# Kernel optimization log

Hardware: AMD Instinct MI355X
Metric: run time of the kernel (lower is better)

The kernel has to match this reference:

```python
import jax, jax.numpy as jnp
import numpy as np

N_WIN = 8      # windows per side (j = i = n_win)
NUM_HEADS = 8
TOPK = 4


def setup_inputs() -> dict:
    key = jax.random.key(0)
    k1, k2 = jax.random.split(key)
    cv_feature = jax.random.normal(k1, (1, 128, 128, 256), dtype=jnp.float32)
    mv_feature = jax.random.normal(k2, (1, 4, 128, 128, 256), dtype=jnp.float32)
    return {"cv_feature": cv_feature, "mv_feature": mv_feature}


def reference(cv_feature, mv_feature):
    n, H, W, C = cv_feature.shape
    v = mv_feature.shape[1]
    j = i = N_WIN
    h, w = H // j, W // i
    p2, w2 = j * i, h * w
    m = NUM_HEADS
    ch = C // m
    scale = C ** (-0.5)  # module uses d_model**-0.5 for both routing and pixel attn

    # window partition: n (j h)(i w) c -> n (j i) h w c
    cv_patch = cv_feature.reshape(n, j, h, i, w, C).transpose(0, 1, 3, 2, 4, 5).reshape(n, p2, h, w, C)
    mv_patch = mv_feature.reshape(n, v, j, h, i, w, C).transpose(0, 1, 2, 4, 3, 5, 6).reshape(n, v, p2, h, w, C)

    q_pix = cv_patch.reshape(n, p2, w2, C)          # n p2 w2 c
    kv_pix = mv_patch.reshape(n, v, p2, w2, C)      # n v p2 w2 c

    # window-level pooled queries/keys (routing is detached in the original)
    q_win = jax.lax.stop_gradient(cv_patch.mean((2, 3)))            # n p2 c
    k_win = jax.lax.stop_gradient(mv_patch.mean((3, 4)))            # n v p2 c
    k_win = k_win.reshape(n, v * p2, C)

    logits = jnp.einsum('npc,nqc->npq', q_win * scale, k_win)       # n p2 (v p2)
    topk_logit, r_idx = jax.lax.top_k(logits, TOPK)                 # n p2 k
    r_weight = jax.nn.softmax(topk_logit, axis=-1)                  # computed, unused (faithful)

    # gather routed KV windows: n p2 k w2 c
    kv_flat = kv_pix.reshape(n, v * p2, w2, C)
    kv_sel = jnp.take_along_axis(kv_flat[:, None], r_idx[:, :, :, None, None], axis=2)

    # split heads
    k_sel = kv_sel.reshape(n, p2, TOPK, w2, m, ch)                  # n p2 k w2 m ch
    q = q_pix.reshape(n, p2, w2, m, ch)                             # n p2 w2 m ch

    attn = jnp.einsum('npqmc,npkwmc->npmqkw', q * scale, k_sel)
    attn = attn.reshape(n, p2, m, w2, TOPK * w2)
    attn = jax.nn.softmax(attn, axis=-1)

    v_sel = k_sel.transpose(0, 1, 4, 2, 3, 5).reshape(n, p2, m, TOPK * w2, ch)
    out = jnp.einsum('npmqt,npmtc->npmqc', attn, v_sel)             # n p2 m w2 ch

    # merge heads + window un-partition: -> n H W C
    out = out.transpose(0, 1, 3, 2, 4).reshape(n, j, i, h, w, C)
    out = out.transpose(0, 1, 3, 2, 4, 5).reshape(n, H, W, C)
    return out
```

## Files before the change

### kernel.cpp

```cpp
#include <hip/hip_runtime.h>
#include <hip/hip_bf16.h>


typedef __attribute__((ext_vector_type(4))) float f32x4;
typedef __attribute__((ext_vector_type(8))) short s16x8;
typedef __attribute__((ext_vector_type(4))) short s16x4;
typedef __attribute__((ext_vector_type(2))) unsigned u32x2;
typedef __attribute__((ext_vector_type(4))) unsigned u32x4;

#define SCALE 0.0625f
#define LOG2E 1.44269504088896340736f

__device__ inline unsigned cvt_pk_bf16(float lo, float hi) {
  unsigned r;
  asm("v_cvt_pk_bf16_f32 %0, %1, %2" : "=v"(r) : "v"(lo), "v"(hi));
  return r;
}

__global__ __launch_bounds__(256) void k_means(const float* __restrict__ cv,
                                               const float* __restrict__ mv,
                                               float* __restrict__ qwin,
                                               float* __restrict__ kwin) {
  __shared__ float sm[4][64];
  int wi = blockIdx.x >> 2, cq = blockIdx.x & 3;
  int pq = threadIdx.x >> 6, cl = threadIdx.x & 63;
  int c = cq * 64 + cl;
  const float* base;
  float* dst;
  if (wi < 64) {
    base = cv + ((size_t)((wi >> 3) * 16) * 128 + (wi & 7) * 16) * 256;
    dst = qwin + wi * 256;
  } else {
    int r = wi - 64;
    base = mv + (size_t)(r >> 6) * (128 * 128 * 256)
         + ((size_t)(((r >> 3) & 7) * 16) * 128 + (r & 7) * 16) * 256;
    dst = kwin + r * 256;
  }
  float s = 0.f;
  for (int k = 0; k < 64; ++k) {
    int px = pq * 64 + k;
    s += base[((px >> 4) * 128 + (px & 15)) * 256 + c];
  }
  sm[pq][cl] = s;
  __syncthreads();
  if (pq == 0)
    dst[c] = (sm[0][cl] + sm[1][cl] + sm[2][cl] + sm[3][cl]) * (1.f / 256.f);
}

__global__ __launch_bounds__(256) void k_route(const float* __restrict__ qwin,
                                               const float* __restrict__ kwin,
                                               int* __restrict__ ridx) {
  __shared__ float qrow[256];
  __shared__ float sv[256];
  __shared__ float wbv[4];
  __shared__ int wbi[4];
  int p = blockIdx.x, t = threadIdx.x;
  qrow[t] = qwin[p * 256 + t] * SCALE;
  __syncthreads();
  const f32x4* kr = reinterpret_cast<const f32x4*>(kwin + t * 256);
  float dot = 0.f;
#pragma unroll 4
  for (int c4 = 0; c4 < 64; ++c4) {
    f32x4 kv = kr[c4];
    dot += qrow[c4 * 4 + 0] * kv[0] + qrow[c4 * 4 + 1] * kv[1]
         + qrow[c4 * 4 + 2] * kv[2] + qrow[c4 * 4 + 3] * kv[3];
  }
  sv[t] = dot;
  __syncthreads();
  for (int k = 0; k < 4; ++k) {
    float v = sv[t];
    int ii = t;
#pragma unroll
    for (int off = 32; off > 0; off >>= 1) {
      float ov = __shfl_down(v, off, 64);
      int oi = __shfl_down(ii, off, 64);
      if (ov > v || (ov == v && oi < ii)) { v = ov; ii = oi; }
    }
    if ((t & 63) == 0) { wbv[t >> 6] = v; wbi[t >> 6] = ii; }
    __syncthreads();
    if (t == 0) {
      float bv = wbv[0]; int bi = wbi[0];
      for (int j = 1; j < 4; ++j)
        if (wbv[j] > bv || (wbv[j] == bv && wbi[j] < bi)) { bv = wbv[j]; bi = wbi[j]; }
      ridx[p * 4 + k] = bi;
      sv[bi] = -3.0e38f;
    }
    __syncthreads();
  }
}

__global__ __launch_bounds__(256, 2) void k_attn(const float* __restrict__ cv,
                                                 const float* __restrict__ mv,
                                                 const int* __restrict__ ridx,
                                                 float* __restrict__ out) {
  __shared__ __align__(16) short kv_lds[256 * 32];
  __shared__ __align__(16) short p_lds[4 * 64 * 32];

  const int tid = threadIdx.x;
  const int lane = tid & 63, wv = tid >> 6;
  const int g = lane >> 4, c16 = lane & 15;
  const int p = blockIdx.x >> 3, m = blockIdx.x & 7;
  const int py = p >> 3, px = p & 7;

  const int4 ridx4 = *reinterpret_cast<const int4*>(ridx + p * 4);

  const float qs = SCALE * LOG2E;
  s16x8 qf[4];
#pragma unroll
  for (int qt = 0; qt < 4; ++qt) {
    const float* qp = cv + ((size_t)((py * 16 + wv * 4 + qt) * 128) + px * 16 + c16) * 256
                         + m * 32 + g * 8;
    f32x4 a = *reinterpret_cast<const f32x4*>(qp);
    f32x4 b = *reinterpret_cast<const f32x4*>(qp + 4);
    union { u32x4 u; s16x8 s; } cu;
    cu.u[0] = cvt_pk_bf16(a[0] * qs, a[1] * qs);
    cu.u[1] = cvt_pk_bf16(a[2] * qs, a[3] * qs);
    cu.u[2] = cvt_pk_bf16(b[0] * qs, b[1] * qs);
    cu.u[3] = cvt_pk_bf16(b[2] * qs, b[3] * qs);
    qf[qt] = cu.s;
  }

  f32x4 accO[4][2];
  float lsum[4];
#pragma unroll
  for (int qt = 0; qt < 4; ++qt) {
    lsum[qt] = 0.f;
    accO[qt][0] = f32x4{0.f, 0.f, 0.f, 0.f};
    accO[qt][1] = f32x4{0.f, 0.f, 0.f, 0.f};
  }
  const f32x4 zf = {0.f, 0.f, 0.f, 0.f};
  short* pw = p_lds + wv * (64 * 32);

  for (int w = 0; w < 4; ++w) {
    if (w) __syncthreads();
    {
      int r = (&ridx4.x)[w];
      const float* srcb = mv + (size_t)(r >> 6) * (128 * 128 * 256)
                        + ((size_t)(((r >> 3) & 7) * 16) * 128 + (r & 7) * 16) * 256 + m * 32;
#pragma unroll
      for (int i = 0; i < 8; ++i) {
        int u = i * 256 + tid;
        int pxl = u >> 3, quad = u & 7;
        f32x4 d = *reinterpret_cast<const f32x4*>(
            srcb + ((pxl >> 4) * 128 + (pxl & 15)) * 256 + quad * 4);
        u32x2 pk;
        pk[0] = cvt_pk_bf16(d[0], d[1]);
        pk[1] = cvt_pk_bf16(d[2], d[3]);
        int off = (pxl >> 2) * 128 + (quad >> 2) * 64 + (pxl & 3) * 16 + (quad & 3) * 4;
        *reinterpret_cast<u32x2*>(&kv_lds[off]) = pk;
      }
    }
    __syncthreads();

    for (int s = 0; s < 8; ++s) {
#pragma unroll
      for (int kt = 0; kt < 2; ++kt) {
        int krow = s * 32 + kt * 16 + c16;
        const s16x8 kf = *reinterpret_cast<const s16x8*>(
            &kv_lds[(krow >> 2) * 128 + (g >> 1) * 64 + (krow & 3) * 16 + (g & 1) * 8]);
#pragma unroll
        for (int qt = 0; qt < 4; ++qt) {
          f32x4 st = __builtin_amdgcn_mfma_f32_16x16x32_bf16(kf, qf[qt], zf, 0, 0, 0);
          float p0 = exp2f(st[0]), p1 = exp2f(st[1]), p2 = exp2f(st[2]), p3 = exp2f(st[3]);
          lsum[qt] += (p0 + p1) + (p2 + p3);
          u32x2 pk;
          pk[0] = cvt_pk_bf16(p0, p1);
          pk[1] = cvt_pk_bf16(p2, p3);
          int q = qt * 16 + c16;
          int slot = (2 * kt + (g >> 1)) ^ (q & 3);
          *reinterpret_cast<u32x2*>(&pw[q * 32 + (slot << 3) + (g & 1) * 4]) = pk;
        }
      }
      asm volatile("s_waitcnt lgkmcnt(0)" ::: "memory");
      __builtin_amdgcn_sched_barrier(0);
      s16x8 V0, V1;
      {
        int r0 = s * 8 + 2 * g;
#pragma unroll
        for (int j = 0; j < 8; ++j) {
          int a = (r0 + (j >> 2)) * 128 + (j & 3) * 16 + c16;
          V0[j] = kv_lds[a];
          V1[j] = kv_lds[a + 64];
        }
      }
#pragma unroll
      for (int qt = 0; qt < 4; ++qt) {
        int q = qt * 16 + c16;
        const s16x8 pf = *reinterpret_cast<const s16x8*>(
            &pw[q * 32 + ((g ^ (q & 3)) << 3)]);
        accO[qt][0] = __builtin_amdgcn_mfma_f32_16x16x32_bf16(V0, pf, accO[qt][0], 0, 0, 0);
        accO[qt][1] = __builtin_amdgcn_mfma_f32_16x16x32_bf16(V1, pf, accO[qt][1], 0, 0, 0);
      }
      asm volatile("" ::: "memory");
    }
  }

#pragma unroll
  for (int qt = 0; qt < 4; ++qt) {
    float l = lsum[qt];
    l += __shfl_xor(l, 16, 64);
    l += __shfl_xor(l, 32, 64);
    float rl = 1.f / l;
#pragma unroll
    for (int mt = 0; mt < 2; ++mt) {
      f32x4 o = accO[qt][mt];
      o[0] *= rl; o[1] *= rl; o[2] *= rl; o[3] *= rl;
      float* op = out + ((size_t)((py * 16 + wv * 4 + qt) * 128) + px * 16 + c16) * 256
                      + m * 32 + mt * 16 + g * 4;
      *reinterpret_cast<f32x4*>(op) = o;
    }
  }
}

extern "C" void kernel_launch(void* const* d_in, const int* in_sizes, int n_in,
                              void* d_out, int out_size, void* d_ws, size_t ws_size,
                              hipStream_t stream) {
  const float* cv = (const float*)d_in[0];
  const float* mv = (const float*)d_in[1];
  float* out = (float*)d_out;

  float* qwin = (float*)d_ws;
  float* kwin = qwin + 64 * 256;
  int* ridx = (int*)(kwin + 256 * 256);

  k_means<<<1280, 256, 0, stream>>>(cv, mv, qwin, kwin);
  k_route<<<64, 256, 0, stream>>>(qwin, kwin, ridx);
  k_attn<<<512, 256, 0, stream>>>(cv, mv, ridx, out);
}
```

Before: 87.04 us.

## Split routed KV windows across two wave groups with LDS merge of partial outputs

The attention kernel now launches 512 threads per block. Two groups of four waves each process two of the four routed KV windows in parallel, each using its own LDS buffer. Because no running max is used, the partial output accumulators and row sums simply add. Group 1 writes them to swizzled LDS and group 0 combines, normalizes and stores. This halves the sequential window loop per block and raises parallelism, at the cost of doubled LDS use and an extra merge step. It also swaps exp2f for the hardware exp2 builtin.

```diff
diff --git a/kernel.cpp b/kernel.cpp
--- a/kernel.cpp
+++ b/kernel.cpp
@@ -16,6 +16,11 @@
   asm("v_cvt_pk_bf16_f32 %0, %1, %2" : "=v"(r) : "v"(lo), "v"(hi));
   return r;
 }
+#if __has_builtin(__builtin_amdgcn_exp2f)
+#define EXP2(x) __builtin_amdgcn_exp2f(x)
+#else
+#define EXP2(x) exp2f(x)
+#endif
 
 __global__ __launch_bounds__(256) void k_means(const float* __restrict__ cv,
                                                const float* __restrict__ mv,
@@ -89,15 +94,16 @@
   }
 }
 
-__global__ __launch_bounds__(256, 2) void k_attn(const float* __restrict__ cv,
+__global__ __launch_bounds__(512, 4) void k_attn(const float* __restrict__ cv,
                                                  const float* __restrict__ mv,
                                                  const int* __restrict__ ridx,
                                                  float* __restrict__ out) {
-  __shared__ __align__(16) short kv_lds[256 * 32];
-  __shared__ __align__(16) short p_lds[4 * 64 * 32];
+  __shared__ __align__(16) short kv_lds[2 * 256 * 32];
+  __shared__ __align__(16) short p_lds[8 * 64 * 32];
 
   const int tid = threadIdx.x;
   const int lane = tid & 63, wv = tid >> 6;
+  const int qw = wv & 3, grp = wv >> 2;
   const int g = lane >> 4, c16 = lane & 15;
   const int p = blockIdx.x >> 3, m = blockIdx.x & 7;
   const int py = p >> 3, px = p & 7;
@@ -108,7 +114,7 @@
   s16x8 qf[4];
 #pragma unroll
   for (int qt = 0; qt < 4; ++qt) {
-    const float* qp = cv + ((size_t)((py * 16 + wv * 4 + qt) * 128) + px * 16 + c16) * 256
+    const float* qp = cv + ((size_t)((py * 16 + qw * 4 + qt) * 128) + px * 16 + c16) * 256
                          + m * 32 + g * 8;
     f32x4 a = *reinterpret_cast<const f32x4*>(qp);
     f32x4 b = *reinterpret_cast<const f32x4*>(qp + 4);
@@ -130,16 +136,18 @@
   }
   const f32x4 zf = {0.f, 0.f, 0.f, 0.f};
   short* pw = p_lds + wv * (64 * 32);
-
-  for (int w = 0; w < 4; ++w) {
-    if (w) __syncthreads();
+  short* kvg = kv_lds + grp * (256 * 32);
+  const int g256 = tid & 255;
+
+  for (int ww = 0; ww < 2; ++ww) {
+    if (ww) __syncthreads();
     {
-      int r = (&ridx4.x)[w];
+      int r = (&ridx4.x)[grp * 2 + ww];
       const float* srcb = mv + (size_t)(r >> 6) * (128 * 128 * 256)
                         + ((size_t)(((r >> 3) & 7) * 16) * 128 + (r & 7) * 16) * 256 + m * 32;
 #pragma unroll
       for (int i = 0; i < 8; ++i) {
-        int u = i * 256 + tid;
+        int u = i * 256 + g256;
         int pxl = u >> 3, quad = u & 7;
         f32x4 d = *reinterpret_cast<const f32x4*>(
             srcb + ((pxl >> 4) * 128 + (pxl & 15)) * 256 + quad * 4);
@@ -147,7 +155,7 @@
         pk[0] = cvt_pk_bf16(d[0], d[1]);
         pk[1] = cvt_pk_bf16(d[2], d[3]);
         int off = (pxl >> 2) * 128 + (quad >> 2) * 64 + (pxl & 3) * 16 + (quad & 3) * 4;
-        *reinterpret_cast<u32x2*>(&kv_lds[off]) = pk;
+        *reinterpret_cast<u32x2*>(&kvg[off]) = pk;
       }
     }
     __syncthreads();
@@ -157,11 +165,11 @@
       for (int kt = 0; kt < 2; ++kt) {
         int krow = s * 32 + kt * 16 + c16;
         const s16x8 kf = *reinterpret_cast<const s16x8*>(
-            &kv_lds[(krow >> 2) * 128 + (g >> 1) * 64 + (krow & 3) * 16 + (g & 1) * 8]);
+            &kvg[(krow >> 2) * 128 + (g >> 1) * 64 + (krow & 3) * 16 + (g & 1) * 8]);
 #pragma unroll
         for (int qt = 0; qt < 4; ++qt) {
           f32x4 st = __builtin_amdgcn_mfma_f32_16x16x32_bf16(kf, qf[qt], zf, 0, 0, 0);
-          float p0 = exp2f(st[0]), p1 = exp2f(st[1]), p2 = exp2f(st[2]), p3 = exp2f(st[3]);
+          float p0 = EXP2(st[0]), p1 = EXP2(st[1]), p2 = EXP2(st[2]), p3 = EXP2(st[3]);
           lsum[qt] += (p0 + p1) + (p2 + p3);
           u32x2 pk;
           pk[0] = cvt_pk_bf16(p0, p1);
@@ -179,8 +187,8 @@
 #pragma unroll
         for (int j = 0; j < 8; ++j) {
           int a = (r0 + (j >> 2)) * 128 + (j & 3) * 16 + c16;
-          V0[j] = kv_lds[a];
-          V1[j] = kv_lds[a + 64];
+          V0[j] = kvg[a];
+          V1[j] = kvg[a + 64];
         }
       }
 #pragma unroll
@@ -195,19 +203,50 @@
     }
   }
 
+  float lred[4];
 #pragma unroll
   for (int qt = 0; qt < 4; ++qt) {
     float l = lsum[qt];
     l += __shfl_xor(l, 16, 64);
     l += __shfl_xor(l, 32, 64);
-    float rl = 1.f / l;
-#pragma unroll
-    for (int mt = 0; mt < 2; ++mt) {
-      f32x4 o = accO[qt][mt];
-      o[0] *= rl; o[1] *= rl; o[2] *= rl; o[3] *= rl;
-      float* op = out + ((size_t)((py * 16 + wv * 4 + qt) * 128) + px * 16 + c16) * 256
-                      + m * 32 + mt * 16 + g * 4;
-      *reinterpret_cast<f32x4*>(op) = o;
+    lred[qt] = l;
+  }
+  __syncthreads();
+  float* mO = reinterpret_cast<float*>(p_lds);
+  float* lbuf = reinterpret_cast<float*>(kv_lds);
+  if (grp == 1) {
+#pragma unroll
+    for (int qt = 0; qt < 4; ++qt) {
+      int q = qt * 16 + c16;
+#pragma unroll
+      for (int mt = 0; mt < 2; ++mt) {
+        unsigned byte = (unsigned)(q * 128 + (mt * 16 + g * 4) * 4);
+        byte ^= (unsigned)((q & 7) << 4);
+        *reinterpret_cast<f32x4*>(
+            reinterpret_cast<char*>(mO + qw * 2048) + byte) = accO[qt][mt];
+      }
+      if (g == 0) lbuf[qw * 64 + q] = lred[qt];
+    }
+  }
+  __syncthreads();
+  if (grp == 0) {
+#pragma unroll
+    for (int qt = 0; qt < 4; ++qt) {
+      int q = qt * 16 + c16;
+      float rl = 1.f / (lred[qt] + lbuf[qw * 64 + q]);
+#pragma unroll
+      for (int mt = 0; mt < 2; ++mt) {
+        unsigned byte = (unsigned)(q * 128 + (mt * 16 + g * 4) * 4);
+        byte ^= (unsigned)((q & 7) << 4);
+        f32x4 po = *reinterpret_cast<const f32x4*>(
+            reinterpret_cast<const char*>(mO + qw * 2048) + byte);
+        f32x4 o = accO[qt][mt];
+        o[0] = (o[0] + po[0]) * rl; o[1] = (o[1] + po[1]) * rl;
+        o[2] = (o[2] + po[2]) * rl; o[3] = (o[3] + po[3]) * rl;
+        float* op = out + ((size_t)((py * 16 + qw * 4 + qt) * 128) + px * 16 + c16) * 256
+                        + m * 32 + mt * 16 + g * 4;
+        *reinterpret_cast<f32x4*>(op) = o;
+      }
     }
   }
 }
@@ -225,5 +264,5 @@
 
   k_means<<<1280, 256, 0, stream>>>(cv, mv, qwin, kwin);
   k_route<<<64, 256, 0, stream>>>(qwin, kwin, ridx);
-  k_attn<<<512, 256, 0, stream>>>(cv, mv, ridx, out);
-}
+  k_attn<<<512, 512, 0, stream>>>(cv, mv, ridx, out);
+}
```

Measured after the change: 96.40 us. 1.11x slower.

## Keep softmax probabilities in registers instead of round-tripping through LDS

Applied to the files above, without the earlier changes.

The attention kernel now builds the P operand for the PV MFMA directly from the QK MFMA output registers. It does this by remapping which key rows feed V0/V1, so the LDS staging buffer, its writes and reads, and the waitcnt/sched barrier all go away. The change also uses the raw hardware exp2 builtin and a software round-to-nearest-even bf16 pack. The aim is to cut LDS traffic and shared memory use, which could raise occupancy, at the cost of more VALU work for the packing and a less precise exp.

```diff
diff --git a/kernel.cpp b/kernel.cpp
--- a/kernel.cpp
+++ b/kernel.cpp
@@ -16,6 +16,18 @@
   asm("v_cvt_pk_bf16_f32 %0, %1, %2" : "=v"(r) : "v"(lo), "v"(hi));
   return r;
 }
+__device__ inline unsigned pk_bf16_rne(float lo, float hi) {
+  unsigned a = __float_as_uint(lo);
+  unsigned b = __float_as_uint(hi);
+  a += 0x7FFFu + ((a >> 16) & 1u);
+  b += 0x7FFFu + ((b >> 16) & 1u);
+  return (a >> 16) | (b & 0xFFFF0000u);
+}
+#if __has_builtin(__builtin_amdgcn_exp2f)
+#define EXP2(x) __builtin_amdgcn_exp2f(x)
+#else
+#define EXP2(x) exp2f(x)
+#endif
 
 __global__ __launch_bounds__(256) void k_means(const float* __restrict__ cv,
                                                const float* __restrict__ mv,
@@ -94,7 +106,6 @@
                                                  const int* __restrict__ ridx,
                                                  float* __restrict__ out) {
   __shared__ __align__(16) short kv_lds[256 * 32];
-  __shared__ __align__(16) short p_lds[4 * 64 * 32];
 
   const int tid = threadIdx.x;
   const int lane = tid & 63, wv = tid >> 6;
@@ -129,7 +140,6 @@
     accO[qt][1] = f32x4{0.f, 0.f, 0.f, 0.f};
   }
   const f32x4 zf = {0.f, 0.f, 0.f, 0.f};
-  short* pw = p_lds + wv * (64 * 32);
 
   for (int w = 0; w < 4; ++w) {
     if (w) __syncthreads();
@@ -153,45 +163,34 @@
     __syncthreads();
 
     for (int s = 0; s < 8; ++s) {
-#pragma unroll
-      for (int kt = 0; kt < 2; ++kt) {
-        int krow = s * 32 + kt * 16 + c16;
-        const s16x8 kf = *reinterpret_cast<const s16x8*>(
-            &kv_lds[(krow >> 2) * 128 + (g >> 1) * 64 + (krow & 3) * 16 + (g & 1) * 8]);
-#pragma unroll
-        for (int qt = 0; qt < 4; ++qt) {
-          f32x4 st = __builtin_amdgcn_mfma_f32_16x16x32_bf16(kf, qf[qt], zf, 0, 0, 0);
-          float p0 = exp2f(st[0]), p1 = exp2f(st[1]), p2 = exp2f(st[2]), p3 = exp2f(st[3]);
-          lsum[qt] += (p0 + p1) + (p2 + p3);
-          u32x2 pk;
-          pk[0] = cvt_pk_bf16(p0, p1);
-          pk[1] = cvt_pk_bf16(p2, p3);
-          int q = qt * 16 + c16;
-          int slot = (2 * kt + (g >> 1)) ^ (q & 3);
-          *reinterpret_cast<u32x2*>(&pw[q * 32 + (slot << 3) + (g & 1) * 4]) = pk;
-        }
+      int kr0 = s * 32 + c16;
+      int kr1 = kr0 + 16;
+      const s16x8 kf0 = *reinterpret_cast<const s16x8*>(
+          &kv_lds[(kr0 >> 2) * 128 + (g >> 1) * 64 + (kr0 & 3) * 16 + (g & 1) * 8]);
+      const s16x8 kf1 = *reinterpret_cast<const s16x8*>(
+          &kv_lds[(kr1 >> 2) * 128 + (g >> 1) * 64 + (kr1 & 3) * 16 + (g & 1) * 8]);
+      s16x8 V0, V1;
+#pragma unroll
+      for (int j = 0; j < 8; ++j) {
+        int a = (s * 8 + (j >> 2) * 4 + g) * 128 + (j & 3) * 16 + c16;
+        V0[j] = kv_lds[a];
+        V1[j] = kv_lds[a + 64];
       }
-      asm volatile("s_waitcnt lgkmcnt(0)" ::: "memory");
-      __builtin_amdgcn_sched_barrier(0);
-      s16x8 V0, V1;
-      {
-        int r0 = s * 8 + 2 * g;
-#pragma unroll
-        for (int j = 0; j < 8; ++j) {
-          int a = (r0 + (j >> 2)) * 128 + (j & 3) * 16 + c16;
-          V0[j] = kv_lds[a];
-          V1[j] = kv_lds[a + 64];
-        }
+#pragma unroll
+      for (int qt = 0; qt < 4; ++qt) {
+        f32x4 sx = __builtin_amdgcn_mfma_f32_16x16x32_bf16(kf0, qf[qt], zf, 0, 0, 0);
+        f32x4 sy = __builtin_amdgcn_mfma_f32_16x16x32_bf16(kf1, qf[qt], zf, 0, 0, 0);
+        float x0 = EXP2(sx[0]), x1 = EXP2(sx[1]), x2 = EXP2(sx[2]), x3 = EXP2(sx[3]);
+        float y0 = EXP2(sy[0]), y1 = EXP2(sy[1]), y2 = EXP2(sy[2]), y3 = EXP2(sy[3]);
+        lsum[qt] += ((x0 + x1) + (x2 + x3)) + ((y0 + y1) + (y2 + y3));
+        union { u32x4 u; s16x8 s; } pb;
+        pb.u[0] = pk_bf16_rne(x0, x1);
+        pb.u[1] = pk_bf16_rne(x2, x3);
+        pb.u[2] = pk_bf16_rne(y0, y1);
+        pb.u[3] = pk_bf16_rne(y2, y3);
+        accO[qt][0] = __builtin_amdgcn_mfma_f32_16x16x32_bf16(V0, pb.s, accO[qt][0], 0, 0, 0);
+        accO[qt][1] = __builtin_amdgcn_mfma_f32_16x16x32_bf16(V1, pb.s, accO[qt][1], 0, 0, 0);
       }
-#pragma unroll
-      for (int qt = 0; qt < 4; ++qt) {
-        int q = qt * 16 + c16;
-        const s16x8 pf = *reinterpret_cast<const s16x8*>(
-            &pw[q * 32 + ((g ^ (q & 3)) << 3)]);
-        accO[qt][0] = __builtin_amdgcn_mfma_f32_16x16x32_bf16(V0, pf, accO[qt][0], 0, 0, 0);
-        accO[qt][1] = __builtin_amdgcn_mfma_f32_16x16x32_bf16(V1, pf, accO[qt][1], 0, 0, 0);
-      }
-      asm volatile("" ::: "memory");
     }
   }
 
```

After: 71.77 us. -17.5%, faster.
